# Optimization experiments

Hardware: AMD Instinct MI355X
Metric: run time of the kernel (lower is better)

The kernel has to match this reference:

```python
import jax, jax.numpy as jnp
import numpy as np

B, S, H = 2, 2048, 2048
NH, NKV, HD = 16, 8, 128
W_BIT, A_BIT = 8, 8
THETA = 10000.0


def fake_quant(x, bits):
    # symmetric per-tensor fake quantization with straight-through rounding
    qmax = float(2 ** (bits - 1) - 1)
    scale = jnp.maximum(jnp.max(jnp.abs(x)) / qmax, jnp.asarray(1e-8, x.dtype))
    q = jnp.clip(jnp.round(x / scale), -qmax - 1.0, qmax) * scale
    return x + jax.lax.stop_gradient(q - x)


def rotate_half(x):
    d = x.shape[-1] // 2
    return jnp.concatenate([-x[..., d:], x[..., :d]], axis=-1)


def rope_cos_sin(position_ids, head_dim, theta, dtype):
    inv_freq = 1.0 / (theta ** (jnp.arange(0, head_dim, 2, dtype=jnp.float32) / head_dim))
    freqs = position_ids.astype(jnp.float32)[..., None] * inv_freq  # [B,S,HD/2]
    emb = jnp.concatenate([freqs, freqs], axis=-1)                   # [B,S,HD]
    return jnp.cos(emb).astype(dtype), jnp.sin(emb).astype(dtype)


def setup_inputs() -> dict:
    key = jax.random.key(0)
    ks = jax.random.split(key, 5)
    sc = 0.02
    return {
        "hidden_states": jax.random.normal(ks[0], (B, S, H), jnp.float32),
        "wq": jax.random.normal(ks[1], (NH * HD, H), jnp.float32) * sc,
        "wk": jax.random.normal(ks[2], (NKV * HD, H), jnp.float32) * sc,
        "wv": jax.random.normal(ks[3], (NKV * HD, H), jnp.float32) * sc,
        "wo": jax.random.normal(ks[4], (H, NH * HD), jnp.float32) * sc,
        "position_ids": jnp.broadcast_to(jnp.arange(S, dtype=jnp.int64), (B, S)),
    }


def reference(hidden_states, wq, wk, wv, wo, position_ids):
    b, s, _ = hidden_states.shape
    x = fake_quant(hidden_states, A_BIT)
    q = jnp.einsum("bsh,oh->bso", x, fake_quant(wq, W_BIT))
    k = jnp.einsum("bsh,oh->bso", x, fake_quant(wk, W_BIT))
    v = jnp.einsum("bsh,oh->bso", x, fake_quant(wv, W_BIT))
    q = q.reshape(b, s, NH, HD).transpose(0, 2, 1, 3)    # [B,NH,S,HD]
    k = k.reshape(b, s, NKV, HD).transpose(0, 2, 1, 3)   # [B,NKV,S,HD]
    v = v.reshape(b, s, NKV, HD).transpose(0, 2, 1, 3)

    cos, sin = rope_cos_sin(position_ids, HD, THETA, hidden_states.dtype)
    cos, sin = cos[:, None], sin[:, None]                # [B,1,S,HD]
    q = q * cos + rotate_half(q) * sin
    k = k * cos + rotate_half(k) * sin

    rep = NH // NKV
    k = jnp.repeat(k, rep, axis=1)                       # [B,NH,S,HD]
    v = jnp.repeat(v, rep, axis=1)

    scores = jnp.einsum("bhqd,bhkd->bhqk", q, k) / np.sqrt(HD)
    causal = jnp.tril(jnp.ones((s, s), bool))
    scores = jnp.where(causal, scores, jnp.asarray(-1e30, scores.dtype))
    probs = jax.nn.softmax(scores, axis=-1)
    attn = jnp.einsum("bhqk,bhkd->bhqd", probs, v)       # [B,NH,S,HD]
    attn = attn.transpose(0, 2, 1, 3).reshape(b, s, NH * HD)

    attn = fake_quant(attn, A_BIT)
    out = jnp.einsum("bso,ho->bsh", attn, fake_quant(wo, W_BIT))
    return out
```

## Files before the change

### kernel.cpp

```cpp
#include <hip/hip_runtime.h>
#include <cstdint>
#include <cstddef>

#define DEVI __device__ __forceinline__

typedef __attribute__((ext_vector_type(8))) short bf16x8;
typedef __attribute__((ext_vector_type(4))) float f32x4;
typedef __attribute__((ext_vector_type(4))) int   i32x4;
typedef unsigned short u16;
typedef unsigned int   u32;

DEVI u16 f2bf(float f) {
  u32 u = __float_as_uint(f);
  u += 0x7FFFu + ((u >> 16) & 1u);
  return (u16)(u >> 16);
}

DEVI void gload16(const void* g, void* l) {
  __builtin_amdgcn_global_load_lds((const __attribute__((address_space(1))) u32*)g,
                                   (__attribute__((address_space(3))) u32*)l, 16, 0, 0);
}

DEVI f32x4 MFMA_BF16(bf16x8 a, bf16x8 b, f32x4 c) {
  return __builtin_amdgcn_mfma_f32_16x16x32_bf16(a, b, c, 0, 0, 0);
}
DEVI i32x4 MFMA_I8(i32x4 a, i32x4 b, i32x4 c) {
  return __builtin_amdgcn_mfma_i32_16x16x64_i8(a, b, c, 0, 0, 0);
}

DEVI float slot_scale(const u32* s) {
  return fmaxf(__uint_as_float(*s) * (1.f / 127.f), 1e-8f);
}

DEVI float fexp2(float x) { return __builtin_amdgcn_exp2f(x); }

__global__ void k_init(const float* __restrict__ hs, const float* __restrict__ wq,
                       const float* __restrict__ wk, const float* __restrict__ wv,
                       const float* __restrict__ wo, float* __restrict__ ct,
                       float* __restrict__ st_, u32* __restrict__ scales) {
  int z = blockIdx.z;
  int tid0 = blockIdx.x * blockDim.x + threadIdx.x;
  int stride = gridDim.x * blockDim.x;
  if (z == 5) {
    for (int t = tid0; t < 131072; t += stride) {
      int s = t >> 6, i = t & 63;
      float invf = expf(-(float)i * (9.210340371976184f / 64.f));
      float ang = (float)s * invf;
      ct[t] = cosf(ang);
      st_[t] = sinf(ang);
    }
    return;
  }
  const float* x = (z == 0) ? hs : (z == 1) ? wq : (z == 2) ? wk : (z == 3) ? wv : wo;
  int n4 = (z == 0) ? 2097152 : (z == 2 || z == 3) ? 524288 : 1048576;
  const f32x4* x4 = (const f32x4*)x;
  float m = 0.f;
  for (int i = tid0; i < n4; i += stride) {
    f32x4 v = x4[i];
    m = fmaxf(m, fmaxf(fmaxf(fabsf(v.x), fabsf(v.y)), fmaxf(fabsf(v.z), fabsf(v.w))));
  }
#pragma unroll
  for (int d = 1; d < 64; d <<= 1) m = fmaxf(m, __shfl_xor(m, d));
  if ((threadIdx.x & 63) == 0) atomicMax(scales + z, __float_as_uint(m));
}

__global__ void k_quant5(const float* __restrict__ hs, const float* __restrict__ wq,
                         const float* __restrict__ wk, const float* __restrict__ wv,
                         const float* __restrict__ wo, char* __restrict__ xq8,
                         char* __restrict__ wqkv8, char* __restrict__ wo8,
                         const u32* __restrict__ scales) {
  int z = blockIdx.z;
  const float* x; char* o; int n4;
  if (z == 0)      { x = hs; o = xq8;                          n4 = 2097152; }
  else if (z == 1) { x = wq; o = wqkv8;                        n4 = 1048576; }
  else if (z == 2) { x = wk; o = wqkv8 + (size_t)2048 * 2048;  n4 = 524288;  }
  else if (z == 3) { x = wv; o = wqkv8 + (size_t)3072 * 2048;  n4 = 524288;  }
  else             { x = wo; o = wo8;                          n4 = 1048576; }
  float inv = 1.f / slot_scale(scales + z);
  int stride = gridDim.x * blockDim.x;
  for (int i = blockIdx.x * blockDim.x + threadIdx.x; i < n4; i += stride) {
    f32x4 v = ((const f32x4*)x)[i];
    int q0 = (int)fminf(fmaxf(rintf(v.x * inv), -128.f), 127.f);
    int q1 = (int)fminf(fmaxf(rintf(v.y * inv), -128.f), 127.f);
    int q2 = (int)fminf(fmaxf(rintf(v.z * inv), -128.f), 127.f);
    int q3 = (int)fminf(fmaxf(rintf(v.w * inv), -128.f), 127.f);
    ((u32*)o)[i] = (u32)(q0 & 255) | ((u32)(q1 & 255) << 8) |
                   ((u32)(q2 & 255) << 16) | ((u32)(q3 & 255) << 24);
  }
}

__global__ void k_quant_i8(const float* __restrict__ x, char* __restrict__ o,
                           int n4, const u32* __restrict__ slot) {
  float inv = 1.f / slot_scale(slot);
  int i = blockIdx.x * blockDim.x + threadIdx.x;
  if (i >= n4) return;
  f32x4 v = ((const f32x4*)x)[i];
  int q0 = (int)fminf(fmaxf(rintf(v.x * inv), -128.f), 127.f);
  int q1 = (int)fminf(fmaxf(rintf(v.y * inv), -128.f), 127.f);
  int q2 = (int)fminf(fmaxf(rintf(v.z * inv), -128.f), 127.f);
  int q3 = (int)fminf(fmaxf(rintf(v.w * inv), -128.f), 127.f);
  ((u32*)o)[i] = (u32)(q0 & 255) | ((u32)(q1 & 255) << 8) |
                 ((u32)(q2 & 255) << 16) | ((u32)(q3 & 255) << 24);
}

__global__ __launch_bounds__(256) void k_gemm_i8(
    const char* __restrict__ A, const char* __restrict__ Bt, float* __restrict__ C,
    int M, int N, int K, const u32* __restrict__ slots, int slotA, int slotB0, int qkvMode) {
  __shared__ __align__(16) char As[128 * 128];
  __shared__ __align__(16) char Bs[128 * 128];
  u32 nwg = gridDim.x * gridDim.y;
  u32 bid = blockIdx.y * gridDim.x + blockIdx.x;
  u32 cpx = nwg >> 3;
  u32 swz = (bid & 7) * cpx + (bid >> 3);
  int m0 = (int)(swz / gridDim.x) * 128, n0 = (int)(swz % gridDim.x) * 128;
  int tid = threadIdx.x, lane = tid & 63, w = tid >> 6;
  int wr = w >> 1, wc = w & 1;
  i32x4 acc[4][4] = {};
  int nkt = K >> 7;
  for (int kt = 0; kt < nkt; ++kt) {
    int k0 = kt << 7;
#pragma unroll
    for (int c = 0; c < 4; ++c) {
      int chunk = w * 4 + c;
      int unit = chunk * 64 + lane;
      int r = unit >> 3, p = unit & 7, u = p ^ (r & 7);
      gload16(A + (size_t)(m0 + r) * K + k0 + u * 16, ((char*)As) + chunk * 1024);
      gload16(Bt + (size_t)(n0 + r) * K + k0 + u * 16, ((char*)Bs) + chunk * 1024);
    }
    asm volatile("s_waitcnt vmcnt(0)" ::: "memory");
    __syncthreads();
#pragma unroll
    for (int ks = 0; ks < 2; ++ks) {
      i32x4 af[4], bfr[4];
#pragma unroll
      for (int mf = 0; mf < 4; ++mf) {
        int r = wr * 64 + mf * 16 + (lane & 15);
        int u = ks * 4 + (lane >> 4);
        af[mf] = *(const i32x4*)(As + r * 128 + ((u ^ (r & 7)) << 4));
      }
#pragma unroll
      for (int nf = 0; nf < 4; ++nf) {
        int r = wc * 64 + nf * 16 + (lane & 15);
        int u = ks * 4 + (lane >> 4);
        bfr[nf] = *(const i32x4*)(Bs + r * 128 + ((u ^ (r & 7)) << 4));
      }
#pragma unroll
      for (int mf = 0; mf < 4; ++mf)
#pragma unroll
        for (int nf = 0; nf < 4; ++nf)
          acc[mf][nf] = MFMA_I8(af[mf], bfr[nf], acc[mf][nf]);
    }
    __syncthreads();
  }
  float sa = slot_scale(slots + slotA);
  int sbi = slotB0 + (qkvMode ? ((n0 >= 3072) ? 2 : (n0 >= 2048) ? 1 : 0) : 0);
  float ss = sa * slot_scale(slots + sbi);
  int rb = m0 + wr * 64, cb = n0 + wc * 64 + (lane & 15);
#pragma unroll
  for (int mf = 0; mf < 4; ++mf)
#pragma unroll
    for (int nf = 0; nf < 4; ++nf)
#pragma unroll
      for (int j = 0; j < 4; ++j)
        C[(size_t)(rb + mf * 16 + (lane >> 4) * 4 + j) * N + cb + nf * 16] =
            (float)acc[mf][nf][j] * ss;
}

__global__ void k_rope(const float* __restrict__ Y, const float* __restrict__ ct,
                       const float* __restrict__ st_, u16* __restrict__ Qh,
                       u16* __restrict__ Kh) {
  int t = blockIdx.x * blockDim.x + threadIdx.x;
  const int QT = 4096 * 16 * 16;
  bool isq = t < QT;
  int tt = isq ? t : t - QT;
  int d4 = tt & 15;
  int hh = isq ? ((tt >> 4) & 15) : ((tt >> 4) & 7);
  int row = isq ? (tt >> 8) : (tt >> 7);
  int s = row & 2047, bb = row >> 11;
  int d = d4 * 4;
  const float* yp = Y + (size_t)row * 4096 + (isq ? hh * 128 : 2048 + hh * 128) + d;
  f32x4 a = *(const f32x4*)yp;
  f32x4 bv = *(const f32x4*)(yp + 64);
  f32x4 c = *(const f32x4*)(ct + s * 64 + d);
  f32x4 sn = *(const f32x4*)(st_ + s * 64 + d);
  f32x4 o0 = a * c - bv * sn;
  f32x4 o1 = bv * c + a * sn;
  u16* dst = isq ? (Qh + ((size_t)(bb * 16 + hh) * 2048 + s) * 128 + d)
                 : (Kh + ((size_t)(bb * 8 + hh) * 2048 + s) * 128 + d);
  *(uint2*)dst = make_uint2((u32)f2bf(o0.x) | ((u32)f2bf(o0.y) << 16),
                            (u32)f2bf(o0.z) | ((u32)f2bf(o0.w) << 16));
  *(uint2*)(dst + 64) = make_uint2((u32)f2bf(o1.x) | ((u32)f2bf(o1.y) << 16),
                                   (u32)f2bf(o1.z) | ((u32)f2bf(o1.w) << 16));
}

__global__ void k_vtrans(const float* __restrict__ Y, u16* __restrict__ Vth) {
  __shared__ u16 tile[64][72];
  int stile = blockIdx.x, dt = blockIdx.y, bh = blockIdx.z;
  int bb = bh >> 3, hk = bh & 7;
  int t = threadIdx.x;
#pragma unroll 4
  for (int i = 0; i < 16; ++i) {
    int e = i * 256 + t;
    int sl = e >> 6, dl = e & 63;
    float v = Y[(size_t)(bb * 2048 + stile * 64 + sl) * 4096 + 3072 + hk * 128 + dt * 64 + dl];
    tile[sl][dl] = f2bf(v);
  }
  __syncthreads();
#pragma unroll 4
  for (int i = 0; i < 16; ++i) {
    int e = i * 256 + t;
    int dl = e >> 6, sl = e & 63;
    Vth[(size_t)((bb * 8 + hk) * 128 + dt * 64 + dl) * 2048 + stile * 64 + sl] = tile[sl][dl];
  }
}

__global__ __launch_bounds__(256, 2) void k_attn(
    const u16* __restrict__ Qh, const u16* __restrict__ Kh, const u16* __restrict__ Vth,
    float* __restrict__ attn, u32* __restrict__ amax_slot) {
  __shared__ __align__(16) u16 Ks[2][64 * 128];
  __shared__ __align__(16) u16 Vts[128 * 64];
  __shared__ __align__(16) u16 Pt[128 * 72];
  int bx = blockIdx.x;
  int qt = (bx & 1) ? (bx >> 1) : (15 - (bx >> 1));
  int h = blockIdx.y, b = blockIdx.z, hk = h >> 1;
  int tid = threadIdx.x, lane = tid & 63, w = tid >> 6;
  int q15 = lane & 15, g4 = lane >> 4;
  const u16* Qbase = Qh + ((size_t)(b * 16 + h) * 2048) * 128;
  const u16* Kbase = Kh + ((size_t)(b * 8 + hk) * 2048) * 128;
  const u16* Vbase = Vth + ((size_t)(b * 8 + hk) * 128) * 2048;
  int qrow0 = qt * 128 + w * 32;
  int qg0 = qrow0 + q15, qg1 = qrow0 + 16 + q15;
  bf16x8 qf0[4], qf1[4];
#pragma unroll
  for (int ks = 0; ks < 4; ++ks) {
    qf0[ks] = *(const bf16x8*)(Qbase + (size_t)qg0 * 128 + ks * 32 + g4 * 8);
    qf1[ks] = *(const bf16x8*)(Qbase + (size_t)qg1 * 128 + ks * 32 + g4 * 8);
  }
  f32x4 o0[8] = {}, o1[8] = {};
  float m0 = -1e30f, m1 = -1e30f, l0 = 0.f, l1 = 0.f;
  const float C2 = 1.4426950408889634f * 0.08838834764831845f;
  int nkv = 2 * qt + 2;

  auto stage_k = [&](int kvb, u16* buf) {
#pragma unroll
    for (int c = 0; c < 4; ++c) {
      int chunk = w * 4 + c;
      int unit = chunk * 64 + lane;
      int rk = unit >> 4, pk = unit & 15, uk = pk ^ (rk & 7);
      gload16(Kbase + (size_t)(kvb + rk) * 128 + uk * 8, ((char*)buf) + chunk * 1024);
    }
  };
  auto stage_v = [&](int kvb) {
#pragma unroll
    for (int c = 0; c < 4; ++c) {
      int chunk = w * 4 + c;
      int unit = chunk * 64 + lane;
      int rv = unit >> 3, pv = unit & 7, uv = pv ^ (rv & 7);
      gload16(Vbase + (size_t)rv * 2048 + kvb + uv * 8, ((char*)Vts) + chunk * 1024);
    }
  };

  stage_k(0, Ks[0]);
  stage_v(0);
  int cur = 0;
  for (int t = 0; t < nkv; ++t) {
    int kvb = t * 64;
    bool more = (t + 1 < nkv);
    if (more) {
      stage_k(kvb + 64, Ks[cur ^ 1]);
      asm volatile("s_waitcnt vmcnt(4)" ::: "memory");
    } else {
      asm volatile("s_waitcnt vmcnt(0)" ::: "memory");
    }
    __builtin_amdgcn_sched_barrier(0);
    __builtin_amdgcn_s_barrier();
    bool active = (kvb <= qrow0 + 31);
    if (active) {
      const char* Kb = (const char*)Ks[cur];
      f32x4 s0[4] = {}, s1[4] = {};
#pragma unroll
      for (int ks = 0; ks < 4; ++ks)
#pragma unroll
        for (int f = 0; f < 4; ++f) {
          int r = f * 16 + q15;
          int u = ks * 4 + g4;
          bf16x8 kf = *(const bf16x8*)(Kb + r * 256 + ((u ^ (r & 7)) << 4));
          s0[f] = MFMA_BF16(kf, qf0[ks], s0[f]);
          s1[f] = MFMA_BF16(kf, qf1[ks], s1[f]);
        }
      bool needMask = (kvb + 63 > qrow0);
      float t0 = -1e30f, t1 = -1e30f;
#pragma unroll
      for (int f = 0; f < 4; ++f)
#pragma unroll
        for (int j = 0; j < 4; ++j) {
          float x0 = s0[f][j] * C2, x1 = s1[f][j] * C2;
          if (needMask) {
            int kvg = kvb + f * 16 + g4 * 4 + j;
            if (kvg > qg0) x0 = -1e30f;
            if (kvg > qg1) x1 = -1e30f;
          }
          s0[f][j] = x0; s1[f][j] = x1;
          t0 = fmaxf(t0, x0); t1 = fmaxf(t1, x1);
        }
      t0 = fmaxf(t0, __shfl_xor(t0, 16)); t0 = fmaxf(t0, __shfl_xor(t0, 32));
      t1 = fmaxf(t1, __shfl_xor(t1, 16)); t1 = fmaxf(t1, __shfl_xor(t1, 32));
      bool nochg = (t0 <= m0 + 8.f) && (t1 <= m1 + 8.f);
      if (!__all(nochg)) {
        float mn0 = fmaxf(m0, t0), mn1 = fmaxf(m1, t1);
        float a0 = fexp2(m0 - mn0), a1 = fexp2(m1 - mn1);
        m0 = mn0; m1 = mn1;
        l0 *= a0; l1 *= a1;
        float al0[4], al1[4];
#pragma unroll
        for (int j = 0; j < 4; ++j) {
          al0[j] = __shfl(a0, g4 * 4 + j);
          al1[j] = __shfl(a1, g4 * 4 + j);
        }
#pragma unroll
        for (int nf = 0; nf < 8; ++nf)
#pragma unroll
          for (int j = 0; j < 4; ++j) {
            o0[nf][j] *= al0[j];
            o1[nf][j] *= al1[j];
          }
      }
      float ts0 = 0.f, ts1 = 0.f;
#pragma unroll
      for (int f = 0; f < 4; ++f)
#pragma unroll
        for (int j = 0; j < 4; ++j) {
          float p0 = fexp2(s0[f][j] - m0), p1 = fexp2(s1[f][j] - m1);
          s0[f][j] = p0; s1[f][j] = p1;
          ts0 += p0; ts1 += p1;
        }
      ts0 += __shfl_xor(ts0, 16); ts0 += __shfl_xor(ts0, 32);
      ts1 += __shfl_xor(ts1, 16); ts1 += __shfl_xor(ts1, 32);
      l0 += ts0; l1 += ts1;
#pragma unroll
      for (int f = 0; f < 4; ++f) {
        *(uint2*)((char*)Pt + (w * 32 + q15) * 144 + (f * 16 + g4 * 4) * 2) =
            make_uint2((u32)f2bf(s0[f][0]) | ((u32)f2bf(s0[f][1]) << 16),
                       (u32)f2bf(s0[f][2]) | ((u32)f2bf(s0[f][3]) << 16));
        *(uint2*)((char*)Pt + (w * 32 + 16 + q15) * 144 + (f * 16 + g4 * 4) * 2) =
            make_uint2((u32)f2bf(s1[f][0]) | ((u32)f2bf(s1[f][1]) << 16),
                       (u32)f2bf(s1[f][2]) | ((u32)f2bf(s1[f][3]) << 16));
      }
#pragma unroll
      for (int ks2 = 0; ks2 < 2; ++ks2) {
        bf16x8 pf0 = *(const bf16x8*)((char*)Pt + (w * 32 + q15) * 144 +
                                      (ks2 * 32 + g4 * 8) * 2);
        bf16x8 pf1 = *(const bf16x8*)((char*)Pt + (w * 32 + 16 + q15) * 144 +
                                      (ks2 * 32 + g4 * 8) * 2);
#pragma unroll
        for (int nf = 0; nf < 8; ++nf) {
          int rv = nf * 16 + q15;
          int u = ks2 * 4 + g4;
          bf16x8 vf = *(const bf16x8*)((const char*)Vts + rv * 128 + ((u ^ (rv & 7)) << 4));
          o0[nf] = MFMA_BF16(pf0, vf, o0[nf]);
          o1[nf] = MFMA_BF16(pf1, vf, o1[nf]);
        }
      }
    }
    __builtin_amdgcn_s_barrier();
    if (more) stage_v(kvb + 64);
    cur ^= 1;
  }
  float i0 = 1.f / l0, i1 = 1.f / l1;
  float iv0[4], iv1[4];
#pragma unroll
  for (int j = 0; j < 4; ++j) {
    iv0[j] = __shfl(i0, g4 * 4 + j);
    iv1[j] = __shfl(i1, g4 * 4 + j);
  }
  float am = 0.f;
  int colb = h * 128 + q15;
#pragma unroll
  for (int nf = 0; nf < 8; ++nf)
#pragma unroll
    for (int j = 0; j < 4; ++j) {
      int r0 = qrow0 + g4 * 4 + j, r1 = qrow0 + 16 + g4 * 4 + j;
      float v0 = o0[nf][j] * iv0[j], v1 = o1[nf][j] * iv1[j];
      am = fmaxf(am, fmaxf(fabsf(v0), fabsf(v1)));
      attn[(size_t)(b * 2048 + r0) * 2048 + colb + nf * 16] = v0;
      attn[(size_t)(b * 2048 + r1) * 2048 + colb + nf * 16] = v1;
    }
#pragma unroll
  for (int d = 1; d < 64; d <<= 1) am = fmaxf(am, __shfl_xor(am, d));
  if (lane == 0) atomicMax(amax_slot, __float_as_uint(am));
}

extern "C" void kernel_launch(void* const* d_in, const int* in_sizes, int n_in,
                              void* d_out, int out_size, void* d_ws, size_t ws_size,
                              hipStream_t stream) {
  const float* hs = (const float*)d_in[0];
  const float* wq = (const float*)d_in[1];
  const float* wk = (const float*)d_in[2];
  const float* wv = (const float*)d_in[3];
  const float* wo = (const float*)d_in[4];
  float* out = (float*)d_out;

  char* ws = (char*)d_ws;
  size_t off = 0;
  u32* scales = (u32*)ws; off += 256;
  char* xq8 = ws + off;   off += (size_t)4096 * 2048;
  char* wqkv8 = ws + off; off += (size_t)4096 * 2048;
  char* wo8 = ws + off;   off += (size_t)2048 * 2048;
  float* Y = (float*)(ws + off);   off += (size_t)4096 * 4096 * 4;
  u16* Qh = (u16*)(ws + off);      off += (size_t)2 * 16 * 2048 * 128 * 2;
  u16* Kh = (u16*)(ws + off);      off += (size_t)2 * 8 * 2048 * 128 * 2;
  u16* Vth = (u16*)(ws + off);     off += (size_t)2 * 8 * 2048 * 128 * 2;
  float* attnb = (float*)(ws + off); off += (size_t)4096 * 2048 * 4;
  char* attn8 = ws + off;          off += (size_t)4096 * 2048;
  float* ctab = (float*)(ws + off); off += (size_t)2048 * 64 * 4;
  float* stab = (float*)(ws + off); off += (size_t)2048 * 64 * 4;

  hipMemsetAsync(scales, 0, 64, stream);

  hipLaunchKernelGGL(k_init, dim3(256, 1, 6), dim3(256), 0, stream,
                     hs, wq, wk, wv, wo, ctab, stab, scales);
  hipLaunchKernelGGL(k_quant5, dim3(512, 1, 5), dim3(256), 0, stream,
                     hs, wq, wk, wv, wo, xq8, wqkv8, wo8, scales);

  hipLaunchKernelGGL(k_gemm_i8, dim3(32, 32), dim3(256), 0, stream,
                     xq8, wqkv8, Y, 4096, 4096, 2048, scales, 0, 1, 1);

  hipLaunchKernelGGL(k_rope, dim3(6144), dim3(256), 0, stream, Y, ctab, stab, Qh, Kh);
  hipLaunchKernelGGL(k_vtrans, dim3(32, 2, 16), dim3(256), 0, stream, Y, Vth);

  hipLaunchKernelGGL(k_attn, dim3(16, 16, 2), dim3(256), 0, stream, Qh, Kh, Vth,
                     attnb, scales + 5);

  hipLaunchKernelGGL(k_quant_i8, dim3(8192), dim3(256), 0, stream, attnb, attn8,
                     2097152, scales + 5);

  hipLaunchKernelGGL(k_gemm_i8, dim3(16, 32), dim3(256), 0, stream,
                     attn8, wo8, out, 4096, 2048, 2048, scales, 5, 4, 0);
}
```

Baseline: 395.1 us.

## Split attention into single-wave blocks loading K/V fragments directly from global

```diff
diff --git a/kernel.cpp b/kernel.cpp
--- a/kernel.cpp
+++ b/kernel.cpp
@@ -214,21 +214,18 @@
   }
 }
 
-__global__ __launch_bounds__(256, 2) void k_attn(
+__global__ __launch_bounds__(64) void k_attn(
     const u16* __restrict__ Qh, const u16* __restrict__ Kh, const u16* __restrict__ Vth,
     float* __restrict__ attn, u32* __restrict__ amax_slot) {
-  __shared__ __align__(16) u16 Ks[2][64 * 128];
-  __shared__ __align__(16) u16 Vts[128 * 64];
-  __shared__ __align__(16) u16 Pt[128 * 72];
-  int bx = blockIdx.x;
-  int qt = (bx & 1) ? (bx >> 1) : (15 - (bx >> 1));
-  int h = blockIdx.y, b = blockIdx.z, hk = h >> 1;
-  int tid = threadIdx.x, lane = tid & 63, w = tid >> 6;
-  int q15 = lane & 15, g4 = lane >> 4;
+  __shared__ __align__(16) u16 Pt[32 * 72];
+  int bid = blockIdx.x;
+  int g = bid & 15, b = g >> 3, hk = g & 7;
+  int r = bid >> 4, h = hk * 2 + (r & 1), qc = r >> 1;
+  int lane = threadIdx.x & 63, q15 = lane & 15, g4 = lane >> 4;
   const u16* Qbase = Qh + ((size_t)(b * 16 + h) * 2048) * 128;
   const u16* Kbase = Kh + ((size_t)(b * 8 + hk) * 2048) * 128;
   const u16* Vbase = Vth + ((size_t)(b * 8 + hk) * 128) * 2048;
-  int qrow0 = qt * 128 + w * 32;
+  int qrow0 = qc * 32;
   int qg0 = qrow0 + q15, qg1 = qrow0 + 16 + q15;
   bf16x8 qf0[4], qf1[4];
 #pragma unroll
@@ -239,132 +236,94 @@
   f32x4 o0[8] = {}, o1[8] = {};
   float m0 = -1e30f, m1 = -1e30f, l0 = 0.f, l1 = 0.f;
   const float C2 = 1.4426950408889634f * 0.08838834764831845f;
-  int nkv = 2 * qt + 2;
-
-  auto stage_k = [&](int kvb, u16* buf) {
-#pragma unroll
-    for (int c = 0; c < 4; ++c) {
-      int chunk = w * 4 + c;
-      int unit = chunk * 64 + lane;
-      int rk = unit >> 4, pk = unit & 15, uk = pk ^ (rk & 7);
-      gload16(Kbase + (size_t)(kvb + rk) * 128 + uk * 8, ((char*)buf) + chunk * 1024);
-    }
-  };
-  auto stage_v = [&](int kvb) {
-#pragma unroll
-    for (int c = 0; c < 4; ++c) {
-      int chunk = w * 4 + c;
-      int unit = chunk * 64 + lane;
-      int rv = unit >> 3, pv = unit & 7, uv = pv ^ (rv & 7);
-      gload16(Vbase + (size_t)rv * 2048 + kvb + uv * 8, ((char*)Vts) + chunk * 1024);
-    }
-  };
-
-  stage_k(0, Ks[0]);
-  stage_v(0);
-  int cur = 0;
+  int nkv = (qc >> 1) + 1;
   for (int t = 0; t < nkv; ++t) {
     int kvb = t * 64;
-    bool more = (t + 1 < nkv);
-    if (more) {
-      stage_k(kvb + 64, Ks[cur ^ 1]);
-      asm volatile("s_waitcnt vmcnt(4)" ::: "memory");
-    } else {
-      asm volatile("s_waitcnt vmcnt(0)" ::: "memory");
-    }
-    __builtin_amdgcn_sched_barrier(0);
-    __builtin_amdgcn_s_barrier();
-    bool active = (kvb <= qrow0 + 31);
-    if (active) {
-      const char* Kb = (const char*)Ks[cur];
-      f32x4 s0[4] = {}, s1[4] = {};
-#pragma unroll
-      for (int ks = 0; ks < 4; ++ks)
-#pragma unroll
-        for (int f = 0; f < 4; ++f) {
-          int r = f * 16 + q15;
-          int u = ks * 4 + g4;
-          bf16x8 kf = *(const bf16x8*)(Kb + r * 256 + ((u ^ (r & 7)) << 4));
-          s0[f] = MFMA_BF16(kf, qf0[ks], s0[f]);
-          s1[f] = MFMA_BF16(kf, qf1[ks], s1[f]);
+    bf16x8 kf[4][4];
+#pragma unroll
+    for (int ks = 0; ks < 4; ++ks)
+#pragma unroll
+      for (int f = 0; f < 4; ++f)
+        kf[ks][f] = *(const bf16x8*)(Kbase + (size_t)(kvb + f * 16 + q15) * 128 +
+                                     ks * 32 + g4 * 8);
+    f32x4 s0[4] = {}, s1[4] = {};
+#pragma unroll
+    for (int ks = 0; ks < 4; ++ks)
+#pragma unroll
+      for (int f = 0; f < 4; ++f) {
+        s0[f] = MFMA_BF16(kf[ks][f], qf0[ks], s0[f]);
+        s1[f] = MFMA_BF16(kf[ks][f], qf1[ks], s1[f]);
+      }
+    bool needMask = (kvb + 63 > qrow0);
+    float t0 = -1e30f, t1 = -1e30f;
+#pragma unroll
+    for (int f = 0; f < 4; ++f)
+#pragma unroll
+      for (int j = 0; j < 4; ++j) {
+        float x0 = s0[f][j] * C2, x1 = s1[f][j] * C2;
+        if (needMask) {
+          int kvg = kvb + f * 16 + g4 * 4 + j;
+          if (kvg > qg0) x0 = -1e30f;
+          if (kvg > qg1) x1 = -1e30f;
         }
-      bool needMask = (kvb + 63 > qrow0);
-      float t0 = -1e30f, t1 = -1e30f;
-#pragma unroll
-      for (int f = 0; f < 4; ++f)
+        s0[f][j] = x0; s1[f][j] = x1;
+        t0 = fmaxf(t0, x0); t1 = fmaxf(t1, x1);
+      }
+    t0 = fmaxf(t0, __shfl_xor(t0, 16)); t0 = fmaxf(t0, __shfl_xor(t0, 32));
+    t1 = fmaxf(t1, __shfl_xor(t1, 16)); t1 = fmaxf(t1, __shfl_xor(t1, 32));
+    bool nochg = (t0 <= m0 + 8.f) && (t1 <= m1 + 8.f);
+    if (!__all(nochg)) {
+      float mn0 = fmaxf(m0, t0), mn1 = fmaxf(m1, t1);
+      float a0 = fexp2(m0 - mn0), a1 = fexp2(m1 - mn1);
+      m0 = mn0; m1 = mn1;
+      l0 *= a0; l1 *= a1;
+      float al0[4], al1[4];
+#pragma unroll
+      for (int j = 0; j < 4; ++j) {
+        al0[j] = __shfl(a0, g4 * 4 + j);
+        al1[j] = __shfl(a1, g4 * 4 + j);
+      }
+#pragma unroll
+      for (int nf = 0; nf < 8; ++nf)
 #pragma unroll
         for (int j = 0; j < 4; ++j) {
-          float x0 = s0[f][j] * C2, x1 = s1[f][j] * C2;
-          if (needMask) {
-            int kvg = kvb + f * 16 + g4 * 4 + j;
-            if (kvg > qg0) x0 = -1e30f;
-            if (kvg > qg1) x1 = -1e30f;
-          }
-          s0[f][j] = x0; s1[f][j] = x1;
-          t0 = fmaxf(t0, x0); t1 = fmaxf(t1, x1);
+          o0[nf][j] *= al0[j];
+          o1[nf][j] *= al1[j];
         }
-      t0 = fmaxf(t0, __shfl_xor(t0, 16)); t0 = fmaxf(t0, __shfl_xor(t0, 32));
-      t1 = fmaxf(t1, __shfl_xor(t1, 16)); t1 = fmaxf(t1, __shfl_xor(t1, 32));
-      bool nochg = (t0 <= m0 + 8.f) && (t1 <= m1 + 8.f);
-      if (!__all(nochg)) {
-        float mn0 = fmaxf(m0, t0), mn1 = fmaxf(m1, t1);
-        float a0 = fexp2(m0 - mn0), a1 = fexp2(m1 - mn1);
-        m0 = mn0; m1 = mn1;
-        l0 *= a0; l1 *= a1;
-        float al0[4], al1[4];
-#pragma unroll
-        for (int j = 0; j < 4; ++j) {
-          al0[j] = __shfl(a0, g4 * 4 + j);
-          al1[j] = __shfl(a1, g4 * 4 + j);
-        }
-#pragma unroll
-        for (int nf = 0; nf < 8; ++nf)
-#pragma unroll
-          for (int j = 0; j < 4; ++j) {
-            o0[nf][j] *= al0[j];
-            o1[nf][j] *= al1[j];
-          }
-      }
-      float ts0 = 0.f, ts1 = 0.f;
-#pragma unroll
-      for (int f = 0; f < 4; ++f)
-#pragma unroll
-        for (int j = 0; j < 4; ++j) {
-          float p0 = fexp2(s0[f][j] - m0), p1 = fexp2(s1[f][j] - m1);
-          s0[f][j] = p0; s1[f][j] = p1;
-          ts0 += p0; ts1 += p1;
-        }
-      ts0 += __shfl_xor(ts0, 16); ts0 += __shfl_xor(ts0, 32);
-      ts1 += __shfl_xor(ts1, 16); ts1 += __shfl_xor(ts1, 32);
-      l0 += ts0; l1 += ts1;
-#pragma unroll
-      for (int f = 0; f < 4; ++f) {
-        *(uint2*)((char*)Pt + (w * 32 + q15) * 144 + (f * 16 + g4 * 4) * 2) =
-            make_uint2((u32)f2bf(s0[f][0]) | ((u32)f2bf(s0[f][1]) << 16),
-                       (u32)f2bf(s0[f][2]) | ((u32)f2bf(s0[f][3]) << 16));
-        *(uint2*)((char*)Pt + (w * 32 + 16 + q15) * 144 + (f * 16 + g4 * 4) * 2) =
-            make_uint2((u32)f2bf(s1[f][0]) | ((u32)f2bf(s1[f][1]) << 16),
-                       (u32)f2bf(s1[f][2]) | ((u32)f2bf(s1[f][3]) << 16));
-      }
-#pragma unroll
-      for (int ks2 = 0; ks2 < 2; ++ks2) {
-        bf16x8 pf0 = *(const bf16x8*)((char*)Pt + (w * 32 + q15) * 144 +
-                                      (ks2 * 32 + g4 * 8) * 2);
-        bf16x8 pf1 = *(const bf16x8*)((char*)Pt + (w * 32 + 16 + q15) * 144 +
-                                      (ks2 * 32 + g4 * 8) * 2);
-#pragma unroll
-        for (int nf = 0; nf < 8; ++nf) {
-          int rv = nf * 16 + q15;
-          int u = ks2 * 4 + g4;
-          bf16x8 vf = *(const bf16x8*)((const char*)Vts + rv * 128 + ((u ^ (rv & 7)) << 4));
-          o0[nf] = MFMA_BF16(pf0, vf, o0[nf]);
-          o1[nf] = MFMA_BF16(pf1, vf, o1[nf]);
-        }
-      }
-    }
-    __builtin_amdgcn_s_barrier();
-    if (more) stage_v(kvb + 64);
-    cur ^= 1;
+    }
+    float ts0 = 0.f, ts1 = 0.f;
+#pragma unroll
+    for (int f = 0; f < 4; ++f)
+#pragma unroll
+      for (int j = 0; j < 4; ++j) {
+        float p0 = fexp2(s0[f][j] - m0), p1 = fexp2(s1[f][j] - m1);
+        s0[f][j] = p0; s1[f][j] = p1;
+        ts0 += p0; ts1 += p1;
+      }
+    ts0 += __shfl_xor(ts0, 16); ts0 += __shfl_xor(ts0, 32);
+    ts1 += __shfl_xor(ts1, 16); ts1 += __shfl_xor(ts1, 32);
+    l0 += ts0; l1 += ts1;
+#pragma unroll
+    for (int f = 0; f < 4; ++f) {
+      *(uint2*)((char*)Pt + q15 * 144 + (f * 16 + g4 * 4) * 2) =
+          make_uint2((u32)f2bf(s0[f][0]) | ((u32)f2bf(s0[f][1]) << 16),
+                     (u32)f2bf(s0[f][2]) | ((u32)f2bf(s0[f][3]) << 16));
+      *(uint2*)((char*)Pt + (16 + q15) * 144 + (f * 16 + g4 * 4) * 2) =
+          make_uint2((u32)f2bf(s1[f][0]) | ((u32)f2bf(s1[f][1]) << 16),
+                     (u32)f2bf(s1[f][2]) | ((u32)f2bf(s1[f][3]) << 16));
+    }
+#pragma unroll
+    for (int ks2 = 0; ks2 < 2; ++ks2) {
+      bf16x8 pf0 = *(const bf16x8*)((char*)Pt + q15 * 144 + (ks2 * 32 + g4 * 8) * 2);
+      bf16x8 pf1 = *(const bf16x8*)((char*)Pt + (16 + q15) * 144 + (ks2 * 32 + g4 * 8) * 2);
+#pragma unroll
+      for (int nf = 0; nf < 8; ++nf) {
+        bf16x8 vf = *(const bf16x8*)(Vbase + (size_t)(nf * 16 + q15) * 2048 +
+                                     kvb + ks2 * 32 + g4 * 8);
+        o0[nf] = MFMA_BF16(pf0, vf, o0[nf]);
+        o1[nf] = MFMA_BF16(pf1, vf, o1[nf]);
+      }
+    }
   }
   float i0 = 1.f / l0, i1 = 1.f / l1;
   float iv0[4], iv1[4];
@@ -428,7 +387,7 @@
   hipLaunchKernelGGL(k_rope, dim3(6144), dim3(256), 0, stream, Y, ctab, stab, Qh, Kh);
   hipLaunchKernelGGL(k_vtrans, dim3(32, 2, 16), dim3(256), 0, stream, Y, Vth);
 
-  hipLaunchKernelGGL(k_attn, dim3(16, 16, 2), dim3(256), 0, stream, Qh, Kh, Vth,
+  hipLaunchKernelGGL(k_attn, dim3(2048), dim3(64), 0, stream, Qh, Kh, Vth,
                      attnb, scales + 5);
 
   hipLaunchKernelGGL(k_quant_i8, dim3(8192), dim3(256), 0, stream, attnb, attn8,
```

Measured after the change: 537.2 us. +35.9%, slower.

## Pair causal q-tiles per attention block and stage V through registers

Applied to the files above, without the earlier changes.

```diff
diff --git a/kernel.cpp b/kernel.cpp
--- a/kernel.cpp
+++ b/kernel.cpp
@@ -220,27 +220,19 @@
   __shared__ __align__(16) u16 Ks[2][64 * 128];
   __shared__ __align__(16) u16 Vts[128 * 64];
   __shared__ __align__(16) u16 Pt[128 * 72];
-  int bx = blockIdx.x;
-  int qt = (bx & 1) ? (bx >> 1) : (15 - (bx >> 1));
-  int h = blockIdx.y, b = blockIdx.z, hk = h >> 1;
+  int bid = blockIdx.x;
+  int hk = bid & 7, b = (bid >> 3) & 1;
+  int r = bid >> 4, hpar = r & 1, p = r >> 1;
+  int h = hk * 2 + hpar;
   int tid = threadIdx.x, lane = tid & 63, w = tid >> 6;
   int q15 = lane & 15, g4 = lane >> 4;
   const u16* Qbase = Qh + ((size_t)(b * 16 + h) * 2048) * 128;
   const u16* Kbase = Kh + ((size_t)(b * 8 + hk) * 2048) * 128;
   const u16* Vbase = Vth + ((size_t)(b * 8 + hk) * 128) * 2048;
-  int qrow0 = qt * 128 + w * 32;
-  int qg0 = qrow0 + q15, qg1 = qrow0 + 16 + q15;
-  bf16x8 qf0[4], qf1[4];
-#pragma unroll
-  for (int ks = 0; ks < 4; ++ks) {
-    qf0[ks] = *(const bf16x8*)(Qbase + (size_t)qg0 * 128 + ks * 32 + g4 * 8);
-    qf1[ks] = *(const bf16x8*)(Qbase + (size_t)qg1 * 128 + ks * 32 + g4 * 8);
-  }
-  f32x4 o0[8] = {}, o1[8] = {};
-  float m0 = -1e30f, m1 = -1e30f, l0 = 0.f, l1 = 0.f;
   const float C2 = 1.4426950408889634f * 0.08838834764831845f;
-  int nkv = 2 * qt + 2;
-
+  float am = 0.f;
+
+  uint4 vreg[4];
   auto stage_k = [&](int kvb, u16* buf) {
 #pragma unroll
     for (int c = 0; c < 4; ++c) {
@@ -250,141 +242,159 @@
       gload16(Kbase + (size_t)(kvb + rk) * 128 + uk * 8, ((char*)buf) + chunk * 1024);
     }
   };
-  auto stage_v = [&](int kvb) {
+  auto load_v = [&](int kvb) {
 #pragma unroll
     for (int c = 0; c < 4; ++c) {
       int chunk = w * 4 + c;
       int unit = chunk * 64 + lane;
       int rv = unit >> 3, pv = unit & 7, uv = pv ^ (rv & 7);
-      gload16(Vbase + (size_t)rv * 2048 + kvb + uv * 8, ((char*)Vts) + chunk * 1024);
+      vreg[c] = *(const uint4*)(Vbase + (size_t)rv * 2048 + kvb + uv * 8);
     }
   };
-
-  stage_k(0, Ks[0]);
-  stage_v(0);
-  int cur = 0;
-  for (int t = 0; t < nkv; ++t) {
-    int kvb = t * 64;
-    bool more = (t + 1 < nkv);
-    if (more) {
-      stage_k(kvb + 64, Ks[cur ^ 1]);
-      asm volatile("s_waitcnt vmcnt(4)" ::: "memory");
-    } else {
-      asm volatile("s_waitcnt vmcnt(0)" ::: "memory");
-    }
-    __builtin_amdgcn_sched_barrier(0);
-    __builtin_amdgcn_s_barrier();
-    bool active = (kvb <= qrow0 + 31);
-    if (active) {
-      const char* Kb = (const char*)Ks[cur];
-      f32x4 s0[4] = {}, s1[4] = {};
-#pragma unroll
-      for (int ks = 0; ks < 4; ++ks)
+  auto write_v = [&]() {
+#pragma unroll
+    for (int c = 0; c < 4; ++c)
+      *(uint4*)((char*)Vts + (w * 4 + c) * 1024 + lane * 16) = vreg[c];
+  };
+
+  for (int sub = 0; sub < 2; ++sub) {
+    int qt = sub ? 15 - p : p;
+    int qrow0 = qt * 128 + w * 32;
+    int qg0 = qrow0 + q15, qg1 = qrow0 + 16 + q15;
+    bf16x8 qf0[4], qf1[4];
+#pragma unroll
+    for (int ks = 0; ks < 4; ++ks) {
+      qf0[ks] = *(const bf16x8*)(Qbase + (size_t)qg0 * 128 + ks * 32 + g4 * 8);
+      qf1[ks] = *(const bf16x8*)(Qbase + (size_t)qg1 * 128 + ks * 32 + g4 * 8);
+    }
+    f32x4 o0[8] = {}, o1[8] = {};
+    float m0 = -1e30f, m1 = -1e30f, l0 = 0.f, l1 = 0.f;
+    int nkv = 2 * qt + 2;
+    stage_k(0, Ks[0]);
+    load_v(0);
+    __syncthreads();
+    write_v();
+    __syncthreads();
+    int cur = 0;
+    for (int t = 0; t < nkv; ++t) {
+      int kvb = t * 64;
+      bool more = (t + 1 < nkv);
+      if (more) {
+        stage_k(kvb + 64, Ks[cur ^ 1]);
+        load_v(kvb + 64);
+      }
+      bool active = (kvb <= qrow0 + 31);
+      if (active) {
+        const char* Kb = (const char*)Ks[cur];
+        f32x4 s0[4] = {}, s1[4] = {};
+#pragma unroll
+        for (int ks = 0; ks < 4; ++ks)
+#pragma unroll
+          for (int f = 0; f < 4; ++f) {
+            int rr = f * 16 + q15;
+            int u = ks * 4 + g4;
+            bf16x8 kf = *(const bf16x8*)(Kb + rr * 256 + ((u ^ (rr & 7)) << 4));
+            s0[f] = MFMA_BF16(kf, qf0[ks], s0[f]);
+            s1[f] = MFMA_BF16(kf, qf1[ks], s1[f]);
+          }
+        bool needMask = (kvb + 63 > qrow0);
+        float t0 = -1e30f, t1 = -1e30f;
+#pragma unroll
+        for (int f = 0; f < 4; ++f)
+#pragma unroll
+          for (int j = 0; j < 4; ++j) {
+            float x0 = s0[f][j] * C2, x1 = s1[f][j] * C2;
+            if (needMask) {
+              int kvg = kvb + f * 16 + g4 * 4 + j;
+              if (kvg > qg0) x0 = -1e30f;
+              if (kvg > qg1) x1 = -1e30f;
+            }
+            s0[f][j] = x0; s1[f][j] = x1;
+            t0 = fmaxf(t0, x0); t1 = fmaxf(t1, x1);
+          }
+        t0 = fmaxf(t0, __shfl_xor(t0, 16)); t0 = fmaxf(t0, __shfl_xor(t0, 32));
+        t1 = fmaxf(t1, __shfl_xor(t1, 16)); t1 = fmaxf(t1, __shfl_xor(t1, 32));
+        bool nochg = (t0 <= m0 + 8.f) && (t1 <= m1 + 8.f);
+        if (!__all(nochg)) {
+          float mn0 = fmaxf(m0, t0), mn1 = fmaxf(m1, t1);
+          float a0 = fexp2(m0 - mn0), a1 = fexp2(m1 - mn1);
+          m0 = mn0; m1 = mn1;
+          l0 *= a0; l1 *= a1;
+          float al0[4], al1[4];
+#pragma unroll
+          for (int j = 0; j < 4; ++j) {
+            al0[j] = __shfl(a0, g4 * 4 + j);
+            al1[j] = __shfl(a1, g4 * 4 + j);
+          }
+#pragma unroll
+          for (int nf = 0; nf < 8; ++nf)
+#pragma unroll
+            for (int j = 0; j < 4; ++j) {
+              o0[nf][j] *= al0[j];
+              o1[nf][j] *= al1[j];
+            }
+        }
+        float ts0 = 0.f, ts1 = 0.f;
+#pragma unroll
+        for (int f = 0; f < 4; ++f)
+#pragma unroll
+          for (int j = 0; j < 4; ++j) {
+            float p0 = fexp2(s0[f][j] - m0), p1 = fexp2(s1[f][j] - m1);
+            s0[f][j] = p0; s1[f][j] = p1;
+            ts0 += p0; ts1 += p1;
+          }
+        ts0 += __shfl_xor(ts0, 16); ts0 += __shfl_xor(ts0, 32);
+        ts1 += __shfl_xor(ts1, 16); ts1 += __shfl_xor(ts1, 32);
+        l0 += ts0; l1 += ts1;
 #pragma unroll
         for (int f = 0; f < 4; ++f) {
-          int r = f * 16 + q15;
-          int u = ks * 4 + g4;
-          bf16x8 kf = *(const bf16x8*)(Kb + r * 256 + ((u ^ (r & 7)) << 4));
-          s0[f] = MFMA_BF16(kf, qf0[ks], s0[f]);
-          s1[f] = MFMA_BF16(kf, qf1[ks], s1[f]);
+          *(uint2*)((char*)Pt + (w * 32 + q15) * 144 + (f * 16 + g4 * 4) * 2) =
+              make_uint2((u32)f2bf(s0[f][0]) | ((u32)f2bf(s0[f][1]) << 16),
+                         (u32)f2bf(s0[f][2]) | ((u32)f2bf(s0[f][3]) << 16));
+          *(uint2*)((char*)Pt + (w * 32 + 16 + q15) * 144 + (f * 16 + g4 * 4) * 2) =
+              make_uint2((u32)f2bf(s1[f][0]) | ((u32)f2bf(s1[f][1]) << 16),
+                         (u32)f2bf(s1[f][2]) | ((u32)f2bf(s1[f][3]) << 16));
         }
-      bool needMask = (kvb + 63 > qrow0);
-      float t0 = -1e30f, t1 = -1e30f;
-#pragma unroll
-      for (int f = 0; f < 4; ++f)
-#pragma unroll
-        for (int j = 0; j < 4; ++j) {
-          float x0 = s0[f][j] * C2, x1 = s1[f][j] * C2;
-          if (needMask) {
-            int kvg = kvb + f * 16 + g4 * 4 + j;
-            if (kvg > qg0) x0 = -1e30f;
-            if (kvg > qg1) x1 = -1e30f;
+#pragma unroll
+        for (int ks2 = 0; ks2 < 2; ++ks2) {
+          bf16x8 pf0 = *(const bf16x8*)((char*)Pt + (w * 32 + q15) * 144 +
+                                        (ks2 * 32 + g4 * 8) * 2);
+          bf16x8 pf1 = *(const bf16x8*)((char*)Pt + (w * 32 + 16 + q15) * 144 +
+                                        (ks2 * 32 + g4 * 8) * 2);
+#pragma unroll
+          for (int nf = 0; nf < 8; ++nf) {
+            int rv = nf * 16 + q15;
+            int u = ks2 * 4 + g4;
+            bf16x8 vf = *(const bf16x8*)((const char*)Vts + rv * 128 + ((u ^ (rv & 7)) << 4));
+            o0[nf] = MFMA_BF16(pf0, vf, o0[nf]);
+            o1[nf] = MFMA_BF16(pf1, vf, o1[nf]);
           }
-          s0[f][j] = x0; s1[f][j] = x1;
-          t0 = fmaxf(t0, x0); t1 = fmaxf(t1, x1);
-        }
-      t0 = fmaxf(t0, __shfl_xor(t0, 16)); t0 = fmaxf(t0, __shfl_xor(t0, 32));
-      t1 = fmaxf(t1, __shfl_xor(t1, 16)); t1 = fmaxf(t1, __shfl_xor(t1, 32));
-      bool nochg = (t0 <= m0 + 8.f) && (t1 <= m1 + 8.f);
-      if (!__all(nochg)) {
-        float mn0 = fmaxf(m0, t0), mn1 = fmaxf(m1, t1);
-        float a0 = fexp2(m0 - mn0), a1 = fexp2(m1 - mn1);
-        m0 = mn0; m1 = mn1;
-        l0 *= a0; l1 *= a1;
-        float al0[4], al1[4];
-#pragma unroll
-        for (int j = 0; j < 4; ++j) {
-          al0[j] = __shfl(a0, g4 * 4 + j);
-          al1[j] = __shfl(a1, g4 * 4 + j);
-        }
-#pragma unroll
-        for (int nf = 0; nf < 8; ++nf)
-#pragma unroll
-          for (int j = 0; j < 4; ++j) {
-            o0[nf][j] *= al0[j];
-            o1[nf][j] *= al1[j];
-          }
-      }
-      float ts0 = 0.f, ts1 = 0.f;
-#pragma unroll
-      for (int f = 0; f < 4; ++f)
-#pragma unroll
-        for (int j = 0; j < 4; ++j) {
-          float p0 = fexp2(s0[f][j] - m0), p1 = fexp2(s1[f][j] - m1);
-          s0[f][j] = p0; s1[f][j] = p1;
-          ts0 += p0; ts1 += p1;
-        }
-      ts0 += __shfl_xor(ts0, 16); ts0 += __shfl_xor(ts0, 32);
-      ts1 += __shfl_xor(ts1, 16); ts1 += __shfl_xor(ts1, 32);
-      l0 += ts0; l1 += ts1;
-#pragma unroll
-      for (int f = 0; f < 4; ++f) {
-        *(uint2*)((char*)Pt + (w * 32 + q15) * 144 + (f * 16 + g4 * 4) * 2) =
-            make_uint2((u32)f2bf(s0[f][0]) | ((u32)f2bf(s0[f][1]) << 16),
-                       (u32)f2bf(s0[f][2]) | ((u32)f2bf(s0[f][3]) << 16));
-        *(uint2*)((char*)Pt + (w * 32 + 16 + q15) * 144 + (f * 16 + g4 * 4) * 2) =
-            make_uint2((u32)f2bf(s1[f][0]) | ((u32)f2bf(s1[f][1]) << 16),
-                       (u32)f2bf(s1[f][2]) | ((u32)f2bf(s1[f][3]) << 16));
-      }
-#pragma unroll
-      for (int ks2 = 0; ks2 < 2; ++ks2) {
-        bf16x8 pf0 = *(const bf16x8*)((char*)Pt + (w * 32 + q15) * 144 +
-                                      (ks2 * 32 + g4 * 8) * 2);
-        bf16x8 pf1 = *(const bf16x8*)((char*)Pt + (w * 32 + 16 + q15) * 144 +
-                                      (ks2 * 32 + g4 * 8) * 2);
-#pragma unroll
-        for (int nf = 0; nf < 8; ++nf) {
-          int rv = nf * 16 + q15;
-          int u = ks2 * 4 + g4;
-          bf16x8 vf = *(const bf16x8*)((const char*)Vts + rv * 128 + ((u ^ (rv & 7)) << 4));
-          o0[nf] = MFMA_BF16(pf0, vf, o0[nf]);
-          o1[nf] = MFMA_BF16(pf1, vf, o1[nf]);
         }
       }
-    }
-    __builtin_amdgcn_s_barrier();
-    if (more) stage_v(kvb + 64);
-    cur ^= 1;
-  }
-  float i0 = 1.f / l0, i1 = 1.f / l1;
-  float iv0[4], iv1[4];
-#pragma unroll
-  for (int j = 0; j < 4; ++j) {
-    iv0[j] = __shfl(i0, g4 * 4 + j);
-    iv1[j] = __shfl(i1, g4 * 4 + j);
-  }
-  float am = 0.f;
-  int colb = h * 128 + q15;
-#pragma unroll
-  for (int nf = 0; nf < 8; ++nf)
+      __syncthreads();
+      if (more) write_v();
+      __syncthreads();
+      cur ^= 1;
+    }
+    float i0 = 1.f / l0, i1 = 1.f / l1;
+    float iv0[4], iv1[4];
 #pragma unroll
     for (int j = 0; j < 4; ++j) {
-      int r0 = qrow0 + g4 * 4 + j, r1 = qrow0 + 16 + g4 * 4 + j;
-      float v0 = o0[nf][j] * iv0[j], v1 = o1[nf][j] * iv1[j];
-      am = fmaxf(am, fmaxf(fabsf(v0), fabsf(v1)));
-      attn[(size_t)(b * 2048 + r0) * 2048 + colb + nf * 16] = v0;
-      attn[(size_t)(b * 2048 + r1) * 2048 + colb + nf * 16] = v1;
-    }
+      iv0[j] = __shfl(i0, g4 * 4 + j);
+      iv1[j] = __shfl(i1, g4 * 4 + j);
+    }
+    int colb = h * 128 + q15;
+#pragma unroll
+    for (int nf = 0; nf < 8; ++nf)
+#pragma unroll
+      for (int j = 0; j < 4; ++j) {
+        int r0 = qrow0 + g4 * 4 + j, r1 = qrow0 + 16 + g4 * 4 + j;
+        float v0 = o0[nf][j] * iv0[j], v1 = o1[nf][j] * iv1[j];
+        am = fmaxf(am, fmaxf(fabsf(v0), fabsf(v1)));
+        attn[(size_t)(b * 2048 + r0) * 2048 + colb + nf * 16] = v0;
+        attn[(size_t)(b * 2048 + r1) * 2048 + colb + nf * 16] = v1;
+      }
+  }
 #pragma unroll
   for (int d = 1; d < 64; d <<= 1) am = fmaxf(am, __shfl_xor(am, d));
   if (lane == 0) atomicMax(amax_slot, __float_as_uint(am));
@@ -428,7 +438,7 @@
   hipLaunchKernelGGL(k_rope, dim3(6144), dim3(256), 0, stream, Y, ctab, stab, Qh, Kh);
   hipLaunchKernelGGL(k_vtrans, dim3(32, 2, 16), dim3(256), 0, stream, Y, Vth);
 
-  hipLaunchKernelGGL(k_attn, dim3(16, 16, 2), dim3(256), 0, stream, Qh, Kh, Vth,
+  hipLaunchKernelGGL(k_attn, dim3(256), dim3(256), 0, stream, Qh, Kh, Vth,
                      attnb, scales + 5);
 
   hipLaunchKernelGGL(k_quant_i8, dim3(8192), dim3(256), 0, stream, attnb, attn8,
```

After: 410.6 us. 3.9% more time.
